# Optimization experiments

Measured on AMD Instinct MI355X. Metric: run time of the kernel, lower is better.

The kernel has to match this reference:

```python
import jax, jax.numpy as jnp
import numpy as np

H = 8          # num_attention_heads
E = 768        # hidden_size
D = E // H     # attention_head_size = 96
LN_EPS = 1e-5


def setup_inputs() -> dict:
    key = jax.random.key(0)
    ks = jax.random.split(key, 12)
    B, S = 2, 2048
    inp = {
        "hidden_states": jax.random.normal(ks[0], (B, S, E), jnp.float32),
        "distance_matrix": jax.random.uniform(ks[1], (B, S, S), jnp.float32),
        "angle_matrix": jax.random.uniform(ks[2], (B, S, S), jnp.float32),
        "attention_mask": jnp.ones((B, S), jnp.float32),
        # Linear params, stored [in, out] so y = x @ W + b
        "Wq": jax.random.normal(ks[3], (E, E), jnp.float32) * 0.02,
        "bq": jnp.zeros((E,), jnp.float32),
        "Wk": jax.random.normal(ks[4], (E, E), jnp.float32) * 0.02,
        "bk": jnp.zeros((E,), jnp.float32),
        "Wv": jax.random.normal(ks[5], (E, E), jnp.float32) * 0.02,
        "bv": jnp.zeros((E,), jnp.float32),
        # distance_embedding / angle_embedding: Linear(1,1) -> scalar w,b
        "dist_w": jax.random.normal(ks[6], (), jnp.float32) * 0.5,
        "dist_b": jnp.zeros((), jnp.float32),
        "ang_w": jax.random.normal(ks[7], (), jnp.float32) * 0.5,
        "ang_b": jnp.zeros((), jnp.float32),
        "Wo": jax.random.normal(ks[8], (E, E), jnp.float32) * 0.02,
        "bo": jnp.zeros((E,), jnp.float32),
        "ln_gamma": jnp.ones((E,), jnp.float32),
        "ln_beta": jnp.zeros((E,), jnp.float32),
    }
    return inp


def _attention(hidden_states, distance_matrix, angle_matrix, attention_mask,
               Wq, bq, Wk, bk, Wv, bv, dist_w, dist_b, ang_w, ang_b,
               Wo, bo, ln_gamma, ln_beta):
    B, S, _ = hidden_states.shape
    # project and split heads -> [B, H, S, D]
    def heads(x):
        return x.reshape(B, S, H, D).transpose(0, 2, 1, 3)
    q = heads(hidden_states @ Wq + bq)
    k = heads(hidden_states @ Wk + bk)
    v = heads(hidden_states @ Wv + bv)

    scores = jnp.einsum("bhqd,bhkd->bhqk", q, k) / jnp.sqrt(jnp.float32(D))
    # fused pairwise biases, broadcast over heads
    bias = (dist_w * distance_matrix + dist_b) + (ang_w * angle_matrix + ang_b)
    scores = scores + bias[:, None, :, :]
    # additive mask: mask is [B, S] over key dim
    scores = scores + ((1.0 - attention_mask) * -10000.0)[:, None, None, :]

    probs = jax.nn.softmax(scores, axis=-1)  # dropout is identity at eval
    ctx = jnp.einsum("bhqk,bhkd->bhqd", probs, v)
    ctx = ctx.transpose(0, 2, 1, 3).reshape(B, S, E)

    out = ctx @ Wo + bo  # output dropout identity at eval
    res = out + hidden_states
    mu = jnp.mean(res, axis=-1, keepdims=True)
    var = jnp.var(res, axis=-1, keepdims=True)
    out = (res - mu) * jax.lax.rsqrt(var + LN_EPS) * ln_gamma + ln_beta
    return out, probs


def reference(hidden_states, distance_matrix, angle_matrix, attention_mask,
              Wq, bq, Wk, bk, Wv, bv, dist_w, dist_b, ang_w, ang_b,
              Wo, bo, ln_gamma, ln_beta):
    return _attention(hidden_states, distance_matrix, angle_matrix, attention_mask,
                      Wq, bq, Wk, bk, Wv, bv, dist_w, dist_b, ang_w, ang_b,
                      Wo, bo, ln_gamma, ln_beta)
```

## Files before the change

### kernel.cpp

```cpp
#include <hip/hip_runtime.h>
#include <math.h>

#define S_LEN 2048
#define BATCH 2
#define EMB 768
#define NH 8
#define HD 96
#define NTOK (BATCH*S_LEN)
#define RSQRT_D 0.10206207261596575f

typedef unsigned short u16;
typedef __attribute__((ext_vector_type(8))) short bf16x8;
typedef __attribute__((ext_vector_type(4))) float f32x4;

#define MFMA16(a,b,c) __builtin_amdgcn_mfma_f32_16x16x32_bf16(a,b,c,0,0,0)

__device__ __forceinline__ u16 f2bf(float f){
    unsigned u = __float_as_uint(f);
    return (u16)((u + 0x7fffu + ((u>>16)&1u)) >> 16);
}
__device__ __forceinline__ float bf2f(unsigned u){
    return __uint_as_float(u << 16);
}

union U16x8 { u16 u[8]; float4 f4; };
union U16x4 { u16 u[4]; uint2 v2; };

__global__ __launch_bounds__(256) void cvt_bf16_kernel(
    const float* __restrict__ src, u16* __restrict__ dst, int n4)
{
    int i = blockIdx.x * 256 + threadIdx.x;
    if (i < n4) {
        float4 v = ((const float4*)src)[i];
        U16x4 o;
        o.u[0] = f2bf(v.x); o.u[1] = f2bf(v.y); o.u[2] = f2bf(v.z); o.u[3] = f2bf(v.w);
        *(uint2*)(dst + (size_t)i*4) = o.v2;
    }
}

__global__ __launch_bounds__(256) void transcvt_kernel(
    const float* __restrict__ W, u16* __restrict__ Wt)
{
    __shared__ float T[64][65];
    const int t = threadIdx.x;
    const int k0 = blockIdx.y * 64, n0 = blockIdx.x * 64;
    #pragma unroll
    for (int i = 0; i < 4; ++i) {
        int idx = t + 256*i;
        int r = idx >> 4, c4 = idx & 15;
        float4 v = *(const float4*)(W + (size_t)(k0 + r)*EMB + n0 + c4*4);
        T[r][c4*4+0] = v.x; T[r][c4*4+1] = v.y; T[r][c4*4+2] = v.z; T[r][c4*4+3] = v.w;
    }
    __syncthreads();
    #pragma unroll
    for (int i = 0; i < 2; ++i) {
        int idx = t + 256*i;
        int n = idx >> 3, c = idx & 7;
        U16x8 o;
        #pragma unroll
        for (int e = 0; e < 8; ++e) o.u[e] = f2bf(T[c*8+e][n]);
        *(float4*)(Wt + (size_t)(n0 + n)*EMB + k0 + c*8) = o.f4;
    }
}

__global__ __launch_bounds__(256) void qkv_mfma_kernel(
    const u16* __restrict__ hsb,
    const u16* __restrict__ WqT, const float* __restrict__ bq,
    const u16* __restrict__ WkT, const float* __restrict__ bk,
    const u16* __restrict__ WvT, const float* __restrict__ bv,
    u16* __restrict__ qo, u16* __restrict__ ko, u16* __restrict__ vo)
{
    const u16* Wt; const float* bias; u16* out;
    if (blockIdx.z == 0)      { Wt = WqT; bias = bq; out = qo; }
    else if (blockIdx.z == 1) { Wt = WkT; bias = bk; out = ko; }
    else                      { Wt = WvT; bias = bv; out = vo; }

    __shared__ __align__(16) u16 As[64*64];
    __shared__ __align__(16) u16 Bs[64*64];
    const int tid = threadIdx.x;
    const int w = tid >> 6, lane = tid & 63, lh = lane & 15, g = lane >> 4;
    const int wm = w >> 1, wn = w & 1;
    const int row0 = blockIdx.y * 64, col0 = blockIdx.x * 64;

    f32x4 acc[2][2];
    #pragma unroll
    for (int i = 0; i < 2; ++i)
        #pragma unroll
        for (int j = 0; j < 2; ++j) acc[i][j] = (f32x4){0.f,0.f,0.f,0.f};

    for (int k0 = 0; k0 < EMB; k0 += 64) {
        __syncthreads();
        #pragma unroll
        for (int i = 0; i < 2; ++i) {
            int idx = tid + 256*i;
            int r = idx >> 3, c = idx & 7;
            float4 a4 = *(const float4*)(hsb + (size_t)(row0 + r)*EMB + k0 + c*8);
            *(float4*)(As + ((size_t)r*8 + (c ^ (r & 7)))*8) = a4;
            float4 b4 = *(const float4*)(Wt + (size_t)(col0 + r)*EMB + k0 + c*8);
            *(float4*)(Bs + ((size_t)r*8 + (c ^ (r & 7)))*8) = b4;
        }
        __syncthreads();
        bf16x8 af[2][2], bfr[2][2];
        #pragma unroll
        for (int mt = 0; mt < 2; ++mt)
            #pragma unroll
            for (int kk = 0; kk < 2; ++kk) {
                int r = wm*32 + mt*16 + lh;
                af[mt][kk] = *(const bf16x8*)(As + ((size_t)r*8 + ((kk*4+g) ^ (lh & 7)))*8);
            }
        #pragma unroll
        for (int nt = 0; nt < 2; ++nt)
            #pragma unroll
            for (int kk = 0; kk < 2; ++kk) {
                int r = wn*32 + nt*16 + lh;
                bfr[nt][kk] = *(const bf16x8*)(Bs + ((size_t)r*8 + ((kk*4+g) ^ (lh & 7)))*8);
            }
        #pragma unroll
        for (int mt = 0; mt < 2; ++mt)
            #pragma unroll
            for (int nt = 0; nt < 2; ++nt)
                #pragma unroll
                for (int kk = 0; kk < 2; ++kk)
                    acc[mt][nt] = MFMA16(af[mt][kk], bfr[nt][kk], acc[mt][nt]);
    }

    #pragma unroll
    for (int mt = 0; mt < 2; ++mt)
        #pragma unroll
        for (int nt = 0; nt < 2; ++nt)
            #pragma unroll
            for (int r = 0; r < 4; ++r) {
                int tt = row0 + wm*32 + mt*16 + g*4 + r;
                int o  = col0 + wn*32 + nt*16 + lh;
                float val = acc[mt][nt][r] + bias[o];
                int b = tt >> 11, s = tt & (S_LEN - 1);
                int h = o / HD, d = o - h*HD;
                out[((size_t)(b*NH + h)*S_LEN + s)*HD + d] = f2bf(val);
            }
}

__global__ __launch_bounds__(256) void vtrans_kernel(
    const u16* __restrict__ vb, u16* __restrict__ vt)
{
    const int bh = blockIdx.y;
    const int s0 = blockIdx.x * 64;
    __shared__ __align__(16) u16 T[64*96];
    const int t = threadIdx.x;
    #pragma unroll
    for (int i = 0; i < 3; ++i) {
        int idx = t + 256*i;
        int s = idx / 12, c = idx % 12;
        float4 v = *(const float4*)(vb + ((size_t)bh*S_LEN + s0 + s)*HD + c*8);
        *(float4*)(T + ((size_t)s*12 + c)*8) = v;
    }
    __syncthreads();
    #pragma unroll
    for (int i = 0; i < 3; ++i) {
        int idx = t + 256*i;
        int d = idx >> 3, c = idx & 7;
        U16x8 o;
        #pragma unroll
        for (int e = 0; e < 8; ++e) o.u[e] = T[(size_t)(c*8+e)*HD + d];
        *(float4*)(vt + ((size_t)bh*HD + d)*S_LEN + s0 + c*8) = o.f4;
    }
}

__global__ __launch_bounds__(512) void fused_attn_kernel(
    const u16* __restrict__ qbf, const u16* __restrict__ kbf,
    const u16* __restrict__ vt,
    const float* __restrict__ dist, const float* __restrict__ ang,
    const float* __restrict__ mask,
    const float* __restrict__ pdw, const float* __restrict__ pdb,
    const float* __restrict__ paw, const float* __restrict__ pab,
    float* __restrict__ probs, u16* __restrict__ ctxb)
{
    const int bh = blockIdx.y, b = bh >> 3, h = bh & 7;
    const int q0 = blockIdx.x * 32;
    const int tid = threadIdx.x;
    const int lane = tid & 63, w = tid >> 6, lh = lane & 15, g = lane >> 4;
    const int rt = w >> 2;
    const int ct = w & 3;

    __shared__ __align__(16) u16 Us[32*2048];
    __shared__ __align__(16) u16 KV[2*64*96];
    __shared__ __align__(16) float Sfw[8*256];

    u16* Ks0 = KV;
    u16* Ks1 = KV + 6144;

    const int kr_s = tid / 12, kc_s = tid - (tid/12)*12;
    const int kr2_s = (tid+512)/12, kc2_s = (tid+512) - ((tid+512)/12)*12;
    const int vr_s = tid >> 3, vc_s = tid & 7;
    const int vr2_s = (tid+512) >> 3, vc2_s = (tid+512) & 7;

    u16* Qtmp = (u16*)Sfw;
    if (tid < 384) {
        int r = tid / 12, c = tid % 12;
        float4 v = *(const float4*)(qbf + ((size_t)bh*S_LEN + q0 + r)*HD + c*8);
        *(float4*)(Qtmp + ((size_t)r*12 + (c ^ ((r >> 1) & 3)))*8) = v;
    }
    {
        float4 v = *(const float4*)(kbf + ((size_t)bh*S_LEN + kr_s)*HD + kc_s*8);
        *(float4*)(Ks0 + ((size_t)kr_s*12 + (kc_s ^ ((kr_s >> 1) & 3)))*8) = v;
        if (tid < 256) {
            float4 v2 = *(const float4*)(kbf + ((size_t)bh*S_LEN + kr2_s)*HD + kc2_s*8);
            *(float4*)(Ks0 + ((size_t)kr2_s*12 + (kc2_s ^ ((kr2_s >> 1) & 3)))*8) = v2;
        }
    }
    __syncthreads();
    bf16x8 qf[3];
    #pragma unroll
    for (int kk = 0; kk < 3; ++kk) {
        int r = rt*16 + lh;
        qf[kk] = *(const bf16x8*)(Qtmp + ((size_t)r*12 + ((kk*4+g) ^ ((r >> 1) & 3)))*8);
    }
    __syncthreads();

    const float DW = *pdw, AW = *paw, CB = *pdb + *pab;

    const int prow = lane >> 2;
    const int pc   = lane & 3;
    const int erow = rt*16 + prow;
    const size_t drowbase = ((size_t)b*S_LEN + q0 + erow)*S_LEN;
    const int ecol = ct*16 + pc*4;
    const int uoffA = (erow*8 + ((ct*2 + (pc>>1)) ^ (erow & 7)))*8 + (pc & 1)*4;
    float* Sfme = Sfw + w*256;

    float lpart = 0.f;

    for (int kt = 0; kt < 32; ++kt) {
        const u16* Kcur = (kt & 1) ? Ks1 : Ks0;
        u16*       Knxt = (kt & 1) ? Ks0 : Ks1;
        float4 kreg0, kreg1;
        if (kt < 31) {
            kreg0 = *(const float4*)(kbf + ((size_t)bh*S_LEN + (kt+1)*64 + kr_s)*HD + kc_s*8);
            if (tid < 256)
                kreg1 = *(const float4*)(kbf + ((size_t)bh*S_LEN + (kt+1)*64 + kr2_s)*HD + kc2_s*8);
        }
        float4 d4 = *(const float4*)(dist + drowbase + kt*64 + ecol);
        float4 g4 = *(const float4*)(ang  + drowbase + kt*64 + ecol);
        float4 m4 = *(const float4*)(mask + b*S_LEN + kt*64 + ecol);

        f32x4 acc = (f32x4){0.f,0.f,0.f,0.f};
        #pragma unroll
        for (int kk = 0; kk < 3; ++kk) {
            int kr = ct*16 + lh;
            bf16x8 kf = *(const bf16x8*)(Kcur + ((size_t)kr*12 + ((kk*4+g) ^ ((kr >> 1) & 3)))*8);
            acc = MFMA16(qf[kk], kf, acc);
        }
        #pragma unroll
        for (int r = 0; r < 4; ++r)
            Sfme[(g*4 + r)*16 + lh] = acc[r];
        float4 s4 = *(const float4*)&Sfme[prow*16 + pc*4];

        float e0 = __expf(s4.x*RSQRT_D + DW*d4.x + AW*g4.x + CB + (1.f - m4.x) * -10000.f);
        float e1 = __expf(s4.y*RSQRT_D + DW*d4.y + AW*g4.y + CB + (1.f - m4.y) * -10000.f);
        float e2 = __expf(s4.z*RSQRT_D + DW*d4.z + AW*g4.z + CB + (1.f - m4.z) * -10000.f);
        float e3 = __expf(s4.w*RSQRT_D + DW*d4.w + AW*g4.w + CB + (1.f - m4.w) * -10000.f);
        lpart += (e0 + e1) + (e2 + e3);
        U16x4 uk;
        uk.u[0] = f2bf(e0); uk.u[1] = f2bf(e1); uk.u[2] = f2bf(e2); uk.u[3] = f2bf(e3);
        *(uint2*)(Us + (size_t)kt*2048 + uoffA) = uk.v2;

        if (kt < 31) {
            *(float4*)(Knxt + ((size_t)kr_s*12 + (kc_s ^ ((kr_s >> 1) & 3)))*8) = kreg0;
            if (tid < 256)
                *(float4*)(Knxt + ((size_t)kr2_s*12 + (kc2_s ^ ((kr2_s >> 1) & 3)))*8) = kreg1;
        }
        __syncthreads();
    }

    lpart += __shfl_xor(lpart, 1);
    lpart += __shfl_xor(lpart, 2);
    float* mLp = (float*)KV;
    if (pc == 0) mLp[w*16 + prow] = lpart;
    __syncthreads();

    const int trowB = tid >> 4;
    const int c4B   = tid & 15;
    float invl_row = 1.0f / (mLp[((trowB>>4)*4 + 0)*16 + (trowB & 15)]
                           + mLp[((trowB>>4)*4 + 1)*16 + (trowB & 15)]
                           + mLp[((trowB>>4)*4 + 2)*16 + (trowB & 15)]
                           + mLp[((trowB>>4)*4 + 3)*16 + (trowB & 15)]);
    float ils[4];
    #pragma unroll
    for (int r = 0; r < 4; ++r) {
        int rr = g*4 + r;
        ils[r] = 1.0f / (mLp[(rt*4 + 0)*16 + rr] + mLp[(rt*4 + 1)*16 + rr]
                       + mLp[(rt*4 + 2)*16 + rr] + mLp[(rt*4 + 3)*16 + rr]);
    }
    __syncthreads();

    u16* Vs0 = KV;
    u16* Vs1 = KV + 6144;
    {
        float4 v4 = *(const float4*)(vt + ((size_t)bh*HD + vr_s)*S_LEN + vc_s*8);
        *(float4*)(Vs0 + ((size_t)vr_s*8 + (vc_s ^ (vr_s & 7)))*8) = v4;
        if (tid < 256) {
            float4 v42 = *(const float4*)(vt + ((size_t)bh*HD + vr2_s)*S_LEN + vc2_s*8);
            *(float4*)(Vs0 + ((size_t)vr2_s*8 + (vc2_s ^ (vr2_s & 7)))*8) = v42;
        }
    }
    __syncthreads();

    const int uoffB = (trowB*8 + ((c4B >> 1) ^ (trowB & 7)))*8 + (c4B & 1)*4;
    const int dt1 = ct;
    const bool two = (ct < 2);
    const int dt2 = ct + 4;
    f32x4 accA = (f32x4){0.f,0.f,0.f,0.f};
    f32x4 accB = (f32x4){0.f,0.f,0.f,0.f};

    for (int kt = 0; kt < 32; ++kt) {
        const u16* Vcur = (kt & 1) ? Vs1 : Vs0;
        u16*       Vnxt = (kt & 1) ? Vs0 : Vs1;
        float4 vreg0, vreg1;
        if (kt < 31) {
            vreg0 = *(const float4*)(vt + ((size_t)bh*HD + vr_s)*S_LEN + (kt+1)*64 + vc_s*8);
            if (tid < 256)
                vreg1 = *(const float4*)(vt + ((size_t)bh*HD + vr2_s)*S_LEN + (kt+1)*64 + vc2_s*8);
        }
        {
            uint2 uu = *(const uint2*)(Us + (size_t)kt*2048 + uoffB);
            float4 p;
            p.x = bf2f(uu.x & 0xffffu)*invl_row; p.y = bf2f(uu.x >> 16)*invl_row;
            p.z = bf2f(uu.y & 0xffffu)*invl_row; p.w = bf2f(uu.y >> 16)*invl_row;
            *(float4*)(probs + ((size_t)bh*S_LEN + q0 + trowB)*S_LEN + kt*64 + c4B*4) = p;
        }
        int prowB = rt*16 + lh;
        bf16x8 pa[2];
        #pragma unroll
        for (int kk = 0; kk < 2; ++kk)
            pa[kk] = *(const bf16x8*)(Us + (size_t)kt*2048 + ((size_t)prowB*8 + ((kk*4+g) ^ (prowB & 7)))*8);
        #pragma unroll
        for (int kk = 0; kk < 2; ++kk) {
            int vr = dt1*16 + lh;
            bf16x8 vf = *(const bf16x8*)(Vcur + ((size_t)vr*8 + ((kk*4+g) ^ (vr & 7)))*8);
            accA = MFMA16(pa[kk], vf, accA);
        }
        if (two) {
            #pragma unroll
            for (int kk = 0; kk < 2; ++kk) {
                int vr = dt2*16 + lh;
                bf16x8 vf = *(const bf16x8*)(Vcur + ((size_t)vr*8 + ((kk*4+g) ^ (vr & 7)))*8);
                accB = MFMA16(pa[kk], vf, accB);
            }
        }
        if (kt < 31) {
            *(float4*)(Vnxt + ((size_t)vr_s*8 + (vc_s ^ (vr_s & 7)))*8) = vreg0;
            if (tid < 256)
                *(float4*)(Vnxt + ((size_t)vr2_s*8 + (vc2_s ^ (vr2_s & 7)))*8) = vreg1;
        }
        __syncthreads();
    }

    #pragma unroll
    for (int r = 0; r < 4; ++r) {
        int qrow = q0 + rt*16 + g*4 + r;
        ctxb[((size_t)(b*S_LEN + qrow))*EMB + h*HD + dt1*16 + lh] = f2bf(accA[r] * ils[r]);
        if (two)
            ctxb[((size_t)(b*S_LEN + qrow))*EMB + h*HD + dt2*16 + lh] = f2bf(accB[r] * ils[r]);
    }
}

__global__ __launch_bounds__(256) void out_mfma_kernel(
    const u16* __restrict__ ctxb, const u16* __restrict__ WoT,
    const float* __restrict__ bo, const float* __restrict__ hs,
    float* __restrict__ res)
{
    __shared__ __align__(16) u16 As[64*64];
    __shared__ __align__(16) u16 Bs[64*64];
    const int tid = threadIdx.x;
    const int w = tid >> 6, lane = tid & 63, lh = lane & 15, g = lane >> 4;
    const int wm = w >> 1, wn = w & 1;
    const int row0 = blockIdx.y * 64, col0 = blockIdx.x * 64;

    f32x4 acc[2][2];
    #pragma unroll
    for (int i = 0; i < 2; ++i)
        #pragma unroll
        for (int j = 0; j < 2; ++j) acc[i][j] = (f32x4){0.f,0.f,0.f,0.f};

    for (int k0 = 0; k0 < EMB; k0 += 64) {
        __syncthreads();
        #pragma unroll
        for (int i = 0; i < 2; ++i) {
            int idx = tid + 256*i;
            int r = idx >> 3, c = idx & 7;
            float4 a4 = *(const float4*)(ctxb + (size_t)(row0 + r)*EMB + k0 + c*8);
            *(float4*)(As + ((size_t)r*8 + (c ^ (r & 7)))*8) = a4;
            float4 b4 = *(const float4*)(WoT + (size_t)(col0 + r)*EMB + k0 + c*8);
            *(float4*)(Bs + ((size_t)r*8 + (c ^ (r & 7)))*8) = b4;
        }
        __syncthreads();
        bf16x8 af[2][2], bfr[2][2];
        #pragma unroll
        for (int mt = 0; mt < 2; ++mt)
            #pragma unroll
            for (int kk = 0; kk < 2; ++kk) {
                int r = wm*32 + mt*16 + lh;
                af[mt][kk] = *(const bf16x8*)(As + ((size_t)r*8 + ((kk*4+g) ^ (lh & 7)))*8);
            }
        #pragma unroll
        for (int nt = 0; nt < 2; ++nt)
            #pragma unroll
            for (int kk = 0; kk < 2; ++kk) {
                int r = wn*32 + nt*16 + lh;
                bfr[nt][kk] = *(const bf16x8*)(Bs + ((size_t)r*8 + ((kk*4+g) ^ (lh & 7)))*8);
            }
        #pragma unroll
        for (int mt = 0; mt < 2; ++mt)
            #pragma unroll
            for (int nt = 0; nt < 2; ++nt)
                #pragma unroll
                for (int kk = 0; kk < 2; ++kk)
                    acc[mt][nt] = MFMA16(af[mt][kk], bfr[nt][kk], acc[mt][nt]);
    }

    #pragma unroll
    for (int mt = 0; mt < 2; ++mt)
        #pragma unroll
        for (int nt = 0; nt < 2; ++nt)
            #pragma unroll
            for (int r = 0; r < 4; ++r) {
                int tt = row0 + wm*32 + mt*16 + g*4 + r;
                int o  = col0 + wn*32 + nt*16 + lh;
                res[(size_t)tt*EMB + o] = acc[mt][nt][r] + bo[o] + hs[(size_t)tt*EMB + o];
            }
}

__device__ __forceinline__ float block_sum256(float v, float* red) {
    #pragma unroll
    for (int off = 32; off > 0; off >>= 1) v += __shfl_down(v, off);
    int lane = threadIdx.x & 63, w = threadIdx.x >> 6;
    __syncthreads();
    if (lane == 0) red[w] = v;
    __syncthreads();
    return red[0] + red[1] + red[2] + red[3];
}

__global__ __launch_bounds__(256) void ln_kernel(
    float* __restrict__ res, const float* __restrict__ gamma, const float* __restrict__ beta)
{
    const int t = blockIdx.x;
    float* row = res + (size_t)t * EMB;
    const int tid = threadIdx.x;
    __shared__ float red[4];

    float x0 = row[tid], x1 = row[tid + 256], x2 = row[tid + 512];
    float s = block_sum256(x0 + x1 + x2, red);
    float mu = s * (1.0f / (float)EMB);
    float d0 = x0 - mu, d1 = x1 - mu, d2 = x2 - mu;
    float sq = block_sum256(d0*d0 + d1*d1 + d2*d2, red);
    float var = sq * (1.0f / (float)EMB);
    float scale = rsqrtf(var + 1e-5f);

    row[tid]       = d0 * scale * gamma[tid]       + beta[tid];
    row[tid + 256] = d1 * scale * gamma[tid + 256] + beta[tid + 256];
    row[tid + 512] = d2 * scale * gamma[tid + 512] + beta[tid + 512];
}

extern "C" void kernel_launch(void* const* d_in, const int* in_sizes, int n_in,
                              void* d_out, int out_size, void* d_ws, size_t ws_size,
                              hipStream_t stream)
{
    (void)in_sizes; (void)n_in; (void)out_size; (void)ws_size;

    const float* hs   = (const float*)d_in[0];
    const float* dist = (const float*)d_in[1];
    const float* ang  = (const float*)d_in[2];
    const float* mask = (const float*)d_in[3];
    const float* Wq = (const float*)d_in[4];  const float* bq = (const float*)d_in[5];
    const float* Wk = (const float*)d_in[6];  const float* bk = (const float*)d_in[7];
    const float* Wv = (const float*)d_in[8];  const float* bv = (const float*)d_in[9];
    const float* dw = (const float*)d_in[10]; const float* db = (const float*)d_in[11];
    const float* aw = (const float*)d_in[12]; const float* ab = (const float*)d_in[13];
    const float* Wo = (const float*)d_in[14]; const float* bo = (const float*)d_in[15];
    const float* gamma = (const float*)d_in[16]; const float* beta = (const float*)d_in[17];

    float* out   = (float*)d_out;
    float* probs = out + (size_t)NTOK * EMB;

    u16* hsb = (u16*)d_ws;
    u16* WqT = hsb + (size_t)NTOK*EMB;
    u16* WkT = WqT + (size_t)EMB*EMB;
    u16* WvT = WkT + (size_t)EMB*EMB;
    u16* WoT = WvT + (size_t)EMB*EMB;
    u16* qb  = WoT + (size_t)EMB*EMB;
    u16* kb  = qb + (size_t)NTOK*EMB;
    u16* vb  = kb + (size_t)NTOK*EMB;
    u16* vtb = vb + (size_t)NTOK*EMB;
    u16* ctxb = qb;

    cvt_bf16_kernel<<<dim3(NTOK*EMB/4/256), dim3(256), 0, stream>>>(hs, hsb, NTOK*EMB/4);
    transcvt_kernel<<<dim3(12,12), dim3(256), 0, stream>>>(Wq, WqT);
    transcvt_kernel<<<dim3(12,12), dim3(256), 0, stream>>>(Wk, WkT);
    transcvt_kernel<<<dim3(12,12), dim3(256), 0, stream>>>(Wv, WvT);
    transcvt_kernel<<<dim3(12,12), dim3(256), 0, stream>>>(Wo, WoT);

    qkv_mfma_kernel<<<dim3(EMB/64, NTOK/64, 3), dim3(256), 0, stream>>>(
        hsb, WqT, bq, WkT, bk, WvT, bv, qb, kb, vb);

    vtrans_kernel<<<dim3(S_LEN/64, BATCH*NH), dim3(256), 0, stream>>>(vb, vtb);

    fused_attn_kernel<<<dim3(S_LEN/32, BATCH*NH), dim3(512), 0, stream>>>(
        qb, kb, vtb, dist, ang, mask, dw, db, aw, ab, probs, ctxb);

    out_mfma_kernel<<<dim3(EMB/64, NTOK/64), dim3(256), 0, stream>>>(
        ctxb, WoT, bo, hs, out);

    ln_kernel<<<dim3(NTOK), dim3(256), 0, stream>>>(out, gamma, beta);
}
```

Before: 275.3 us.

## Use single-buffered 128-key tiles in fused attention loops

The QK and PV loops now step over 128 keys per iteration instead of 64, giving 16 iterations instead of 32. The K/V shared buffer becomes one 128-row tile rather than a double-buffered pair of 64-row tiles. Each iteration issues twice the MFMA work and global loads per barrier, which is meant to amortise synchronisation and loop overhead. In exchange there is an extra __syncthreads per iteration (two instead of one) before the next tile is written, and global prefetch overlaps less because the shared buffer is no longer double-buffered.

```diff
diff --git a/kernel.cpp b/kernel.cpp
--- a/kernel.cpp
+++ b/kernel.cpp
@@ -182,16 +182,8 @@
     const int ct = w & 3;
 
     __shared__ __align__(16) u16 Us[32*2048];
-    __shared__ __align__(16) u16 KV[2*64*96];
+    __shared__ __align__(16) u16 KV[128*96];
     __shared__ __align__(16) float Sfw[8*256];
-
-    u16* Ks0 = KV;
-    u16* Ks1 = KV + 6144;
-
-    const int kr_s = tid / 12, kc_s = tid - (tid/12)*12;
-    const int kr2_s = (tid+512)/12, kc2_s = (tid+512) - ((tid+512)/12)*12;
-    const int vr_s = tid >> 3, vc_s = tid & 7;
-    const int vr2_s = (tid+512) >> 3, vc2_s = (tid+512) & 7;
 
     u16* Qtmp = (u16*)Sfw;
     if (tid < 384) {
@@ -199,13 +191,12 @@
         float4 v = *(const float4*)(qbf + ((size_t)bh*S_LEN + q0 + r)*HD + c*8);
         *(float4*)(Qtmp + ((size_t)r*12 + (c ^ ((r >> 1) & 3)))*8) = v;
     }
-    {
-        float4 v = *(const float4*)(kbf + ((size_t)bh*S_LEN + kr_s)*HD + kc_s*8);
-        *(float4*)(Ks0 + ((size_t)kr_s*12 + (kc_s ^ ((kr_s >> 1) & 3)))*8) = v;
-        if (tid < 256) {
-            float4 v2 = *(const float4*)(kbf + ((size_t)bh*S_LEN + kr2_s)*HD + kc2_s*8);
-            *(float4*)(Ks0 + ((size_t)kr2_s*12 + (kc2_s ^ ((kr2_s >> 1) & 3)))*8) = v2;
-        }
+    #pragma unroll
+    for (int i = 0; i < 3; ++i) {
+        int idx = tid + 512*i;
+        int r = idx / 12, c = idx - (idx/12)*12;
+        float4 v = *(const float4*)(kbf + ((size_t)bh*S_LEN + r)*HD + c*8);
+        *(float4*)(KV + ((size_t)r*12 + (c ^ ((r >> 1) & 3)))*8) = v;
     }
     __syncthreads();
     bf16x8 qf[3];
@@ -228,44 +219,72 @@
 
     float lpart = 0.f;
 
-    for (int kt = 0; kt < 32; ++kt) {
-        const u16* Kcur = (kt & 1) ? Ks1 : Ks0;
-        u16*       Knxt = (kt & 1) ? Ks0 : Ks1;
-        float4 kreg0, kreg1;
-        if (kt < 31) {
-            kreg0 = *(const float4*)(kbf + ((size_t)bh*S_LEN + (kt+1)*64 + kr_s)*HD + kc_s*8);
-            if (tid < 256)
-                kreg1 = *(const float4*)(kbf + ((size_t)bh*S_LEN + (kt+1)*64 + kr2_s)*HD + kc2_s*8);
-        }
-        float4 d4 = *(const float4*)(dist + drowbase + kt*64 + ecol);
-        float4 g4 = *(const float4*)(ang  + drowbase + kt*64 + ecol);
-        float4 m4 = *(const float4*)(mask + b*S_LEN + kt*64 + ecol);
-
-        f32x4 acc = (f32x4){0.f,0.f,0.f,0.f};
+    for (int kt = 0; kt < 16; ++kt) {
+        float4 kreg[3];
+        if (kt < 15) {
+            #pragma unroll
+            for (int i = 0; i < 3; ++i) {
+                int idx = tid + 512*i;
+                int r = idx / 12, c = idx - (idx/12)*12;
+                kreg[i] = *(const float4*)(kbf + ((size_t)bh*S_LEN + (kt+1)*128 + r)*HD + c*8);
+            }
+        }
+        float4 d40 = *(const float4*)(dist + drowbase + kt*128 + ecol);
+        float4 g40 = *(const float4*)(ang  + drowbase + kt*128 + ecol);
+        float4 d41 = *(const float4*)(dist + drowbase + kt*128 + ecol + 64);
+        float4 g41 = *(const float4*)(ang  + drowbase + kt*128 + ecol + 64);
+        float4 m40 = *(const float4*)(mask + b*S_LEN + kt*128 + ecol);
+        float4 m41 = *(const float4*)(mask + b*S_LEN + kt*128 + ecol + 64);
+
+        f32x4 acc0 = (f32x4){0.f,0.f,0.f,0.f};
+        f32x4 acc1 = (f32x4){0.f,0.f,0.f,0.f};
         #pragma unroll
         for (int kk = 0; kk < 3; ++kk) {
-            int kr = ct*16 + lh;
-            bf16x8 kf = *(const bf16x8*)(Kcur + ((size_t)kr*12 + ((kk*4+g) ^ ((kr >> 1) & 3)))*8);
-            acc = MFMA16(qf[kk], kf, acc);
-        }
-        #pragma unroll
-        for (int r = 0; r < 4; ++r)
-            Sfme[(g*4 + r)*16 + lh] = acc[r];
-        float4 s4 = *(const float4*)&Sfme[prow*16 + pc*4];
-
-        float e0 = __expf(s4.x*RSQRT_D + DW*d4.x + AW*g4.x + CB + (1.f - m4.x) * -10000.f);
-        float e1 = __expf(s4.y*RSQRT_D + DW*d4.y + AW*g4.y + CB + (1.f - m4.y) * -10000.f);
-        float e2 = __expf(s4.z*RSQRT_D + DW*d4.z + AW*g4.z + CB + (1.f - m4.z) * -10000.f);
-        float e3 = __expf(s4.w*RSQRT_D + DW*d4.w + AW*g4.w + CB + (1.f - m4.w) * -10000.f);
-        lpart += (e0 + e1) + (e2 + e3);
-        U16x4 uk;
-        uk.u[0] = f2bf(e0); uk.u[1] = f2bf(e1); uk.u[2] = f2bf(e2); uk.u[3] = f2bf(e3);
-        *(uint2*)(Us + (size_t)kt*2048 + uoffA) = uk.v2;
-
-        if (kt < 31) {
-            *(float4*)(Knxt + ((size_t)kr_s*12 + (kc_s ^ ((kr_s >> 1) & 3)))*8) = kreg0;
-            if (tid < 256)
-                *(float4*)(Knxt + ((size_t)kr2_s*12 + (kc2_s ^ ((kr2_s >> 1) & 3)))*8) = kreg1;
+            int kr0 = ct*16 + lh;
+            bf16x8 kf0 = *(const bf16x8*)(KV + ((size_t)kr0*12 + ((kk*4+g) ^ ((kr0 >> 1) & 3)))*8);
+            acc0 = MFMA16(qf[kk], kf0, acc0);
+            int kr1 = (ct+4)*16 + lh;
+            bf16x8 kf1 = *(const bf16x8*)(KV + ((size_t)kr1*12 + ((kk*4+g) ^ ((kr1 >> 1) & 3)))*8);
+            acc1 = MFMA16(qf[kk], kf1, acc1);
+        }
+        __syncthreads();
+
+        if (kt < 15) {
+            #pragma unroll
+            for (int i = 0; i < 3; ++i) {
+                int idx = tid + 512*i;
+                int r = idx / 12, c = idx - (idx/12)*12;
+                *(float4*)(KV + ((size_t)r*12 + (c ^ ((r >> 1) & 3)))*8) = kreg[i];
+            }
+        }
+
+        {
+            #pragma unroll
+            for (int r = 0; r < 4; ++r)
+                Sfme[(g*4 + r)*16 + lh] = acc0[r];
+            float4 s4 = *(const float4*)&Sfme[prow*16 + pc*4];
+            float e0 = __expf(s4.x*RSQRT_D + DW*d40.x + AW*g40.x + CB + (1.f - m40.x) * -10000.f);
+            float e1 = __expf(s4.y*RSQRT_D + DW*d40.y + AW*g40.y + CB + (1.f - m40.y) * -10000.f);
+            float e2 = __expf(s4.z*RSQRT_D + DW*d40.z + AW*g40.z + CB + (1.f - m40.z) * -10000.f);
+            float e3 = __expf(s4.w*RSQRT_D + DW*d40.w + AW*g40.w + CB + (1.f - m40.w) * -10000.f);
+            lpart += (e0 + e1) + (e2 + e3);
+            U16x4 uk;
+            uk.u[0] = f2bf(e0); uk.u[1] = f2bf(e1); uk.u[2] = f2bf(e2); uk.u[3] = f2bf(e3);
+            *(uint2*)(Us + (size_t)(2*kt)*2048 + uoffA) = uk.v2;
+        }
+        {
+            #pragma unroll
+            for (int r = 0; r < 4; ++r)
+                Sfme[(g*4 + r)*16 + lh] = acc1[r];
+            float4 s4 = *(const float4*)&Sfme[prow*16 + pc*4];
+            float e0 = __expf(s4.x*RSQRT_D + DW*d41.x + AW*g41.x + CB + (1.f - m41.x) * -10000.f);
+            float e1 = __expf(s4.y*RSQRT_D + DW*d41.y + AW*g41.y + CB + (1.f - m41.y) * -10000.f);
+            float e2 = __expf(s4.z*RSQRT_D + DW*d41.z + AW*g41.z + CB + (1.f - m41.z) * -10000.f);
+            float e3 = __expf(s4.w*RSQRT_D + DW*d41.w + AW*g41.w + CB + (1.f - m41.w) * -10000.f);
+            lpart += (e0 + e1) + (e2 + e3);
+            U16x4 uk;
+            uk.u[0] = f2bf(e0); uk.u[1] = f2bf(e1); uk.u[2] = f2bf(e2); uk.u[3] = f2bf(e3);
+            *(uint2*)(Us + (size_t)(2*kt+1)*2048 + uoffA) = uk.v2;
         }
         __syncthreads();
     }
@@ -291,15 +310,12 @@
     }
     __syncthreads();
 
-    u16* Vs0 = KV;
-    u16* Vs1 = KV + 6144;
-    {
-        float4 v4 = *(const float4*)(vt + ((size_t)bh*HD + vr_s)*S_LEN + vc_s*8);
-        *(float4*)(Vs0 + ((size_t)vr_s*8 + (vc_s ^ (vr_s & 7)))*8) = v4;
-        if (tid < 256) {
-            float4 v42 = *(const float4*)(vt + ((size_t)bh*HD + vr2_s)*S_LEN + vc2_s*8);
-            *(float4*)(Vs0 + ((size_t)vr2_s*8 + (vc2_s ^ (vr2_s & 7)))*8) = v42;
-        }
+    #pragma unroll
+    for (int i = 0; i < 3; ++i) {
+        int idx = tid + 512*i;
+        int vr = idx >> 4, c = idx & 15;
+        float4 v4 = *(const float4*)(vt + ((size_t)bh*HD + vr)*S_LEN + c*8);
+        *(float4*)(KV + ((size_t)vr*16 + (c ^ (vr & 7)))*8) = v4;
     }
     __syncthreads();
 
@@ -309,46 +325,58 @@
     const int dt2 = ct + 4;
     f32x4 accA = (f32x4){0.f,0.f,0.f,0.f};
     f32x4 accB = (f32x4){0.f,0.f,0.f,0.f};
-
-    for (int kt = 0; kt < 32; ++kt) {
-        const u16* Vcur = (kt & 1) ? Vs1 : Vs0;
-        u16*       Vnxt = (kt & 1) ? Vs0 : Vs1;
-        float4 vreg0, vreg1;
-        if (kt < 31) {
-            vreg0 = *(const float4*)(vt + ((size_t)bh*HD + vr_s)*S_LEN + (kt+1)*64 + vc_s*8);
-            if (tid < 256)
-                vreg1 = *(const float4*)(vt + ((size_t)bh*HD + vr2_s)*S_LEN + (kt+1)*64 + vc2_s*8);
+    const int prowPV = rt*16 + lh;
+
+    for (int kt = 0; kt < 16; ++kt) {
+        float4 vreg[3];
+        if (kt < 15) {
+            #pragma unroll
+            for (int i = 0; i < 3; ++i) {
+                int idx = tid + 512*i;
+                int vr = idx >> 4, c = idx & 15;
+                vreg[i] = *(const float4*)(vt + ((size_t)bh*HD + vr)*S_LEN + (kt+1)*128 + c*8);
+            }
         }
         {
-            uint2 uu = *(const uint2*)(Us + (size_t)kt*2048 + uoffB);
+            uint2 uu = *(const uint2*)(Us + (size_t)(2*kt)*2048 + uoffB);
             float4 p;
             p.x = bf2f(uu.x & 0xffffu)*invl_row; p.y = bf2f(uu.x >> 16)*invl_row;
             p.z = bf2f(uu.y & 0xffffu)*invl_row; p.w = bf2f(uu.y >> 16)*invl_row;
-            *(float4*)(probs + ((size_t)bh*S_LEN + q0 + trowB)*S_LEN + kt*64 + c4B*4) = p;
-        }
-        int prowB = rt*16 + lh;
-        bf16x8 pa[2];
-        #pragma unroll
-        for (int kk = 0; kk < 2; ++kk)
-            pa[kk] = *(const bf16x8*)(Us + (size_t)kt*2048 + ((size_t)prowB*8 + ((kk*4+g) ^ (prowB & 7)))*8);
-        #pragma unroll
-        for (int kk = 0; kk < 2; ++kk) {
+            *(float4*)(probs + ((size_t)bh*S_LEN + q0 + trowB)*S_LEN + kt*128 + c4B*4) = p;
+            uu = *(const uint2*)(Us + (size_t)(2*kt+1)*2048 + uoffB);
+            p.x = bf2f(uu.x & 0xffffu)*invl_row; p.y = bf2f(uu.x >> 16)*invl_row;
+            p.z = bf2f(uu.y & 0xffffu)*invl_row; p.w = bf2f(uu.y >> 16)*invl_row;
+            *(float4*)(probs + ((size_t)bh*S_LEN + q0 + trowB)*S_LEN + kt*128 + 64 + c4B*4) = p;
+        }
+        bf16x8 pa[4];
+        #pragma unroll
+        for (int kk = 0; kk < 4; ++kk) {
+            int sub = 2*kt + (kk >> 1);
+            int j = (kk & 1)*4 + g;
+            pa[kk] = *(const bf16x8*)(Us + (size_t)sub*2048 + ((size_t)prowPV*8 + (j ^ (prowPV & 7)))*8);
+        }
+        #pragma unroll
+        for (int kk = 0; kk < 4; ++kk) {
             int vr = dt1*16 + lh;
-            bf16x8 vf = *(const bf16x8*)(Vcur + ((size_t)vr*8 + ((kk*4+g) ^ (vr & 7)))*8);
+            bf16x8 vf = *(const bf16x8*)(KV + ((size_t)vr*16 + ((kk*4+g) ^ (vr & 7)))*8);
             accA = MFMA16(pa[kk], vf, accA);
         }
         if (two) {
             #pragma unroll
-            for (int kk = 0; kk < 2; ++kk) {
+            for (int kk = 0; kk < 4; ++kk) {
                 int vr = dt2*16 + lh;
-                bf16x8 vf = *(const bf16x8*)(Vcur + ((size_t)vr*8 + ((kk*4+g) ^ (vr & 7)))*8);
+                bf16x8 vf = *(const bf16x8*)(KV + ((size_t)vr*16 + ((kk*4+g) ^ (vr & 7)))*8);
                 accB = MFMA16(pa[kk], vf, accB);
             }
         }
-        if (kt < 31) {
-            *(float4*)(Vnxt + ((size_t)vr_s*8 + (vc_s ^ (vr_s & 7)))*8) = vreg0;
-            if (tid < 256)
-                *(float4*)(Vnxt + ((size_t)vr2_s*8 + (vc2_s ^ (vr2_s & 7)))*8) = vreg1;
+        __syncthreads();
+        if (kt < 15) {
+            #pragma unroll
+            for (int i = 0; i < 3; ++i) {
+                int idx = tid + 512*i;
+                int vr = idx >> 4, c = idx & 15;
+                *(float4*)(KV + ((size_t)vr*16 + (c ^ (vr & 7)))*8) = vreg[i];
+            }
         }
         __syncthreads();
     }
```

After: 347.3 us. 26.2% more time.
